# Performance work log

Measured on AMD Instinct MI355X. Metric: run time of the kernel, lower is better.

## Reference

```python
import jax, jax.numpy as jnp
import numpy as np

NUM_SCALES = 4
ENC = 64
KMAX = 16
DT = 0.005  # base_time_constant; original code's (undefined) self.dt interpreted as this


def setup_inputs() -> dict:
    key = jax.random.key(0)
    ks = jax.random.split(key, 5)
    events = jax.random.normal(ks[0], (2, 2, 32, 32, 64), dtype=jnp.float32)
    # matches torch.logspace(-3, -1, num_scales)
    time_constants = jnp.logspace(-3.0, -1.0, NUM_SCALES).astype(jnp.float32)
    temporal_kernels = jax.random.normal(ks[1], (NUM_SCALES, ENC, KMAX), dtype=jnp.float32)
    w1 = jax.random.normal(ks[2], (2 * NUM_SCALES, NUM_SCALES), dtype=jnp.float32) * 0.1
    b1 = jnp.zeros((2 * NUM_SCALES,), dtype=jnp.float32)
    w2 = jax.random.normal(ks[3], (NUM_SCALES, 2 * NUM_SCALES), dtype=jnp.float32) * 0.1
    b2 = jnp.zeros((NUM_SCALES,), dtype=jnp.float32)
    return {"events": events, "time_constants": time_constants,
            "temporal_kernels": temporal_kernels, "w1": w1, "b1": b1, "w2": w2, "b2": b2}


def reference(events, time_constants, temporal_kernels, w1, b1, w2, b2):
    B, C, H, W, T = events.shape
    k = min(KMAX, T)
    # decay kernels per scale: [S, k], normalized to sum 1
    t_idx = jnp.arange(k, dtype=jnp.float32)
    decay = jnp.exp(-t_idx[None, :] * DT / time_constants[:, None])
    decay = decay / decay.sum(axis=-1, keepdims=True)
    # combined learnable kernels: [S, E, k]
    combined = decay[:, None, :] * temporal_kernels[:, :, :k]

    Cf = C * H * W
    # one batched cross-correlation (torch F.conv1d semantics == lax conv, no flip)
    x = events.reshape(B * Cf, 1, T)                       # [B*Cf, 1, T]
    kern = combined.reshape(NUM_SCALES * ENC, 1, k)        # [S*E, 1, k]
    out = jax.lax.conv_general_dilated(
        x, kern, window_strides=(1,), padding=[(k // 2, k // 2)],
        dimension_numbers=("NCH", "OIH", "NCH"))           # [B*Cf, S*E, T+1]
    Tp = out.shape[-1]
    # [B, E, S, Cf, Tp] matching torch stack order (enc at dim1, scale at dim2)
    feats = out.reshape(B, Cf, NUM_SCALES, ENC, Tp).transpose(0, 3, 2, 1, 4)

    # torch .var() is unbiased -> ddof=1
    feature_variance = feats.var(axis=-1, ddof=1).mean(axis=(1, 3))  # [B, S]
    h = jax.nn.relu(feature_variance @ w1.T + b1)
    attn = jax.nn.softmax(h @ w2.T + b2, axis=-1)                    # [B, S]

    encoded = (feats * attn[:, None, :, None, None]).sum(axis=2)     # [B, E, Cf, Tp]
    return encoded
```

## Files before the change

### kernel.cpp

```cpp
#include <hip/hip_runtime.h>

#define CF 2048
#define TT 64
#define TP 65
#define KK 16
#define SS 4
#define EE 64
#define BB 2
#define DT_CONST 0.005f

typedef float f32x4 __attribute__((ext_vector_type(4)));
typedef short bf16x8 __attribute__((ext_vector_type(8)));


__global__ void __launch_bounds__(256, 2) kA_gram(const float* __restrict__ events,
                                                  float* __restrict__ ws) {
    __shared__ float xs[16][97];
    __shared__ float S1L[16][16];
    __shared__ float part[16][136];
    const int tid = threadIdx.x;
    const int bq  = blockIdx.x >> 7;

    {
        const float4* src = reinterpret_cast<const float4*>(
            events + (size_t)blockIdx.x * (16 * TT));
        float4 v = src[tid];
        int r = tid >> 4, c0 = ((tid & 15) << 2) + 8;
        xs[r][c0] = v.x; xs[r][c0+1] = v.y; xs[r][c0+2] = v.z; xs[r][c0+3] = v.w;
        for (int idx = tid; idx < 16 * 33; idx += 256) {
            int rr = idx / 33, k = idx % 33;
            int c = (k < 8) ? k : (k + 64);
            xs[rr][c] = 0.f;
        }
    }
    __syncthreads();

    const int r   = tid >> 4;
    const int lag = tid & 15;

    {
        float s = 0.f;
#pragma unroll
        for (int u = 0; u <= 64; ++u) s += xs[r][lag + u];
        S1L[r][lag] = s;
    }
    __syncthreads();

    {
        const float inv65 = 1.f / 65.f;
        float C = 0.f;
#pragma unroll
        for (int u = 0; u <= 64; ++u) C += xs[r][u] * xs[r][u + lag];
        part[r][lag] = C - S1L[r][0] * S1L[r][lag] * inv65;
#pragma unroll
        for (int d1 = 1; d1 <= 15; ++d1) {
            C += xs[r][64 + d1] * xs[r][64 + d1 + lag]
               - xs[r][d1 - 1]  * xs[r][d1 - 1 + lag];
            if (lag + d1 <= 15) {
                int p = 16 * d1 - ((d1 * (d1 - 1)) >> 1) + lag;
                part[r][p] = C - S1L[r][d1] * S1L[r][d1 + lag] * inv65;
            }
        }
    }
    __syncthreads();

    if (tid < 136) {
        float g = 0.f;
#pragma unroll
        for (int rr = 0; rr < 16; ++rr) g += part[rr][tid];
        ws[((size_t)(bq * 136 + tid)) * 128 + (blockIdx.x & 127)] = g;
    }
}

__global__ void __launch_bounds__(256, 2) kB3_main(
        const float* __restrict__ events, const float* __restrict__ tc,
        const float* __restrict__ tk, const float* __restrict__ w1,
        const float* __restrict__ b1, const float* __restrict__ w2,
        const float* __restrict__ b2, const float* __restrict__ ws,
        float* __restrict__ out) {
    __shared__ float U[5248];
    __shared__ float xs[8 * 97];
    __shared__ __align__(16) unsigned short wkbh[64 * 32];
    __shared__ __align__(16) unsigned short wkbl[64 * 32];
    __shared__ __align__(16) unsigned short BmatTh[80 * 24 + 16];
    __shared__ __align__(16) unsigned short BmatTl[80 * 24 + 16];
    float* Gf    = U;
    float* combL = U + 512;
    float* fvL   = U + 4608;
    const int tid = threadIdx.x;
    const int bid = blockIdx.x;
    const int b   = bid >> 8;

    for (int idx = tid; idx < 8 * 33; idx += 256) {
        int rr = idx / 33, k = idx % 33;
        int c = (k < 8) ? k : (k + 64);
        xs[rr * 97 + c] = 0.f;
    }
    if (tid < 128) {
        float4 v = reinterpret_cast<const float4*>(events + (size_t)bid * 512)[tid];
        int rr = tid >> 4, c0 = ((tid & 15) << 2) + 8;
        xs[rr * 97 + c0] = v.x; xs[rr * 97 + c0 + 1] = v.y;
        xs[rr * 97 + c0 + 2] = v.z; xs[rr * 97 + c0 + 3] = v.w;
    }
    for (int v = tid; v < 272; v += 256) {
        int b2 = (v >= 136) ? 1 : 0;
        int p  = v - b2 * 136;
        int pp = p, d1 = 0;
        while (pp >= KK - d1) { pp -= KK - d1; ++d1; }
        int d2 = d1 + pp;
        const float4* rp = reinterpret_cast<const float4*>(ws + (size_t)v * 128);
        float acc = 0.f;
#pragma unroll
        for (int i = 0; i < 32; ++i) { float4 q = rp[i]; acc += (q.x + q.y) + (q.z + q.w); }
        Gf[(b2 * KK + d1) * KK + d2] = acc;
        Gf[(b2 * KK + d2) * KK + d1] = acc;
    }
    {
        int s = tid >> 6;
        float inv = DT_CONST / tc[s];
        float dk[KK]; float dsum = 0.f;
#pragma unroll
        for (int j = 0; j < KK; ++j) { dk[j] = expf(-(float)j * inv); dsum += dk[j]; }
        float rn = 1.f / dsum;
#pragma unroll
        for (int i = 0; i < 4; ++i) {
            float4 v = reinterpret_cast<const float4*>(tk + tid * KK)[i];
            combL[tid * KK + 4*i + 0] = dk[4*i + 0] * rn * v.x;
            combL[tid * KK + 4*i + 1] = dk[4*i + 1] * rn * v.y;
            combL[tid * KK + 4*i + 2] = dk[4*i + 2] * rn * v.z;
            combL[tid * KK + 4*i + 3] = dk[4*i + 3] * rn * v.w;
        }
    }
    __syncthreads();

    {
        float c[KK];
#pragma unroll
        for (int i = 0; i < 4; ++i) {
            float4 v = reinterpret_cast<const float4*>(combL + tid * KK)[i];
            c[4*i] = v.x; c[4*i+1] = v.y; c[4*i+2] = v.z; c[4*i+3] = v.w;
        }
        float acc0 = 0.f, acc1 = 0.f;
#pragma unroll
        for (int d1 = 0; d1 < KK; ++d1) {
            float cd1 = c[d1];
            float t0 = 0.5f * Gf[d1 * KK + d1] * cd1;
            float t1 = 0.5f * Gf[256 + d1 * KK + d1] * cd1;
#pragma unroll
            for (int d2 = d1 + 1; d2 < KK; ++d2) {
                t0 += Gf[d1 * KK + d2] * c[d2];
                t1 += Gf[256 + d1 * KK + d2] * c[d2];
            }
            acc0 += 2.f * cd1 * t0;
            acc1 += 2.f * cd1 * t1;
        }
#pragma unroll
        for (int sft = 1; sft < 64; sft <<= 1) {
            acc0 += __shfl_xor(acc0, sft, 64);
            acc1 += __shfl_xor(acc1, sft, 64);
        }
        if ((tid & 63) == 0) {
            const float scale = 1.f / 8388608.f;
            fvL[(tid >> 6)]     = acc0 * scale;
            fvL[4 + (tid >> 6)] = acc1 * scale;
        }
    }
    __syncthreads();

    {
        float fv[SS];
#pragma unroll
        for (int s = 0; s < SS; ++s) fv[s] = fvL[b * SS + s];
        float h[8];
#pragma unroll
        for (int i = 0; i < 8; ++i) {
            float a = b1[i];
#pragma unroll
            for (int s = 0; s < SS; ++s) a += fv[s] * w1[i * SS + s];
            h[i] = a > 0.f ? a : 0.f;
        }
        float lg[SS]; float mx = -1e30f;
#pragma unroll
        for (int s = 0; s < SS; ++s) {
            float a = b2[s];
#pragma unroll
            for (int i = 0; i < 8; ++i) a += h[i] * w2[s * 8 + i];
            lg[s] = a; mx = fmaxf(mx, a);
        }
        float se = 0.f;
#pragma unroll
        for (int s = 0; s < SS; ++s) { lg[s] = expf(lg[s] - mx); se += lg[s]; }
        float attn[SS];
#pragma unroll
        for (int s = 0; s < SS; ++s) attn[s] = lg[s] / se;
#pragma unroll
        for (int j = 0; j < 4; ++j) {
            int idx = tid * 4 + j;
            int e = idx >> 4, k2 = idx & 15;
            float a = 0.f;
#pragma unroll
            for (int s = 0; s < SS; ++s)
                a += attn[s] * combL[(s * EE + e) * KK + k2];
            unsigned int bits = __float_as_uint(a);
            unsigned short hh = (unsigned short)(bits >> 16);
            float hf = __uint_as_float(((unsigned int)hh) << 16);
            unsigned short ll = (unsigned short)(__float_as_uint(a - hf) >> 16);
            wkbh[e * 32 + k2] = hh;      wkbl[e * 32 + k2] = ll;
            wkbh[e * 32 + 16 + k2] = 0;  wkbl[e * 32 + 16 + k2] = 0;
        }
    }
    __syncthreads();

    const int w   = tid >> 6;
    const int l   = tid & 63;
    const int llo = l & 15, lhi = l >> 4;
    bf16x8 Ah = *reinterpret_cast<const bf16x8*>(&wkbh[(w * 16 + llo) * 32 + 8 * lhi]);
    bf16x8 Al = *reinterpret_cast<const bf16x8*>(&wkbl[(w * 16 + llo) * 32 + 8 * lhi]);
    float* stage = U;
    const size_t obase0 = (size_t)b * 8519680 + (size_t)(bid & 255) * 520;

#pragma unroll 1
    for (int cf = 0; cf < 8; ++cf) {
        for (int idx = tid; idx < 1280; idx += 256) {
            int t = idx >> 4, k2 = idx & 15;
            float x = xs[cf * 97 + t + k2];
            unsigned int bits = __float_as_uint(x);
            unsigned short hh = (unsigned short)(bits >> 16);
            float hf = __uint_as_float(((unsigned int)hh) << 16);
            unsigned short ll = (unsigned short)(__float_as_uint(x - hf) >> 16);
            BmatTh[t * 24 + k2] = hh;
            BmatTl[t * 24 + k2] = ll;
        }
        __syncthreads();
#pragma unroll
        for (int nt = 0; nt < 5; ++nt) {
            bf16x8 Bh = *reinterpret_cast<const bf16x8*>(
                &BmatTh[(nt * 16 + llo) * 24 + 8 * lhi]);
            bf16x8 Bl = *reinterpret_cast<const bf16x8*>(
                &BmatTl[(nt * 16 + llo) * 24 + 8 * lhi]);
            f32x4 acc = {0.f, 0.f, 0.f, 0.f};
            acc = __builtin_amdgcn_mfma_f32_16x16x32_bf16(Al, Bh, acc, 0, 0, 0);
            acc = __builtin_amdgcn_mfma_f32_16x16x32_bf16(Ah, Bl, acc, 0, 0, 0);
            acc = __builtin_amdgcn_mfma_f32_16x16x32_bf16(Ah, Bh, acc, 0, 0, 0);
#pragma unroll
            for (int i = 0; i < 4; ++i)
                stage[(w * 16 + lhi * 4 + i) * 82 + nt * 16 + llo] = acc[i];
        }
        __syncthreads();
        {
            const size_t ob = obase0 + (size_t)cf * 65;
            int q = tid >> 6, t = tid & 63;
#pragma unroll
            for (int kk = 0; kk < 16; ++kk) {
                int e = q * 16 + kk;
                out[ob + (size_t)e * 133120 + t] = stage[e * 82 + t];
            }
            if (tid < 64) out[ob + (size_t)tid * 133120 + 64] = stage[tid * 82 + 64];
        }
        __syncthreads();
    }
}

extern "C" void kernel_launch(void* const* d_in, const int* in_sizes, int n_in,
                              void* d_out, int out_size, void* d_ws, size_t ws_size,
                              hipStream_t stream) {
    const float* events = (const float*)d_in[0];
    const float* tc     = (const float*)d_in[1];
    const float* tk     = (const float*)d_in[2];
    const float* w1     = (const float*)d_in[3];
    const float* b1     = (const float*)d_in[4];
    const float* w2     = (const float*)d_in[5];
    const float* b2     = (const float*)d_in[6];
    float* out = (float*)d_out;
    float* ws  = (float*)d_ws;

    hipLaunchKernelGGL(kA_gram,  dim3(256), dim3(256), 0, stream, events, ws);
    hipLaunchKernelGGL(kB3_main, dim3(512), dim3(256), 0, stream,
                       events, tc, tk, w1, b1, w2, b2, ws, out);
}
```

Before: 36.78 us.

## Split attention MLP into single-block kernel and spread conv over more blocks

Moves the Gram reduction, variance, MLP, softmax and attention-weighted kernel computation out of the main conv kernel into a single-block kernel. That kernel writes the bf16 hi/lo weight matrices to the workspace, so it runs once instead of being repeated in each of 512 blocks. The conv kernel now uses 2048 small blocks of two rows each and writes MFMA results straight to global memory instead of staging them through LDS. The Gram kernel doubles its thread count and splits each lag sum across lane pairs. This adds a third launch and a serial one-block kernel, and the direct stores are less coalesced.

```diff
diff --git a/kernel.cpp b/kernel.cpp
--- a/kernel.cpp
+++ b/kernel.cpp
@@ -1,8 +1,5 @@
 #include <hip/hip_runtime.h>
 
-#define CF 2048
-#define TT 64
-#define TP 65
 #define KK 16
 #define SS 4
 #define EE 64
@@ -12,53 +9,66 @@
 typedef float f32x4 __attribute__((ext_vector_type(4)));
 typedef short bf16x8 __attribute__((ext_vector_type(8)));
 
-
-__global__ void __launch_bounds__(256, 2) kA_gram(const float* __restrict__ events,
+#define WS_WK_F 34816
+
+__global__ void __launch_bounds__(512, 1) kA_gram(const float* __restrict__ events,
                                                   float* __restrict__ ws) {
     __shared__ float xs[16][97];
     __shared__ float S1L[16][16];
     __shared__ float part[16][136];
     const int tid = threadIdx.x;
-    const int bq  = blockIdx.x >> 7;
-
-    {
+
+    if (tid < 256) {
         const float4* src = reinterpret_cast<const float4*>(
-            events + (size_t)blockIdx.x * (16 * TT));
+            events + (size_t)blockIdx.x * 1024);
         float4 v = src[tid];
         int r = tid >> 4, c0 = ((tid & 15) << 2) + 8;
         xs[r][c0] = v.x; xs[r][c0+1] = v.y; xs[r][c0+2] = v.z; xs[r][c0+3] = v.w;
-        for (int idx = tid; idx < 16 * 33; idx += 256) {
-            int rr = idx / 33, k = idx % 33;
-            int c = (k < 8) ? k : (k + 64);
-            xs[rr][c] = 0.f;
-        }
-    }
-    __syncthreads();
-
-    const int r   = tid >> 4;
-    const int lag = tid & 15;
+    }
+    for (int idx = tid; idx < 16 * 33; idx += 512) {
+        int rr = idx / 33, k = idx % 33;
+        xs[rr][(k < 8) ? k : (k + 64)] = 0.f;
+    }
+    __syncthreads();
+
+    const int r   = tid >> 5;
+    const int c   = tid & 31;
+    const int lag = c >> 1;
+    const int h   = c & 1;
+    const int off = h * 33;
+    const float inv65 = 1.f / 65.f;
 
     {
         float s = 0.f;
 #pragma unroll
-        for (int u = 0; u <= 64; ++u) s += xs[r][lag + u];
-        S1L[r][lag] = s;
-    }
-    __syncthreads();
-
-    {
-        const float inv65 = 1.f / 65.f;
+        for (int j = 0; j < 32; ++j) s += xs[r][lag + off + j];
+        if (!h) s += xs[r][lag + 32];
+        s += __shfl_xor(s, 1, 64);
+        if (!h) S1L[r][lag] = s;
+    }
+    __syncthreads();
+
+    {
         float C = 0.f;
 #pragma unroll
-        for (int u = 0; u <= 64; ++u) C += xs[r][u] * xs[r][u + lag];
-        part[r][lag] = C - S1L[r][0] * S1L[r][lag] * inv65;
+        for (int j = 0; j < 32; ++j) C += xs[r][off + j] * xs[r][off + j + lag];
+        if (!h) C += xs[r][32] * xs[r][32 + lag];
+        {
+            float Ct = C + __shfl_xor(C, 1, 64);
+            if (!h) part[r][lag] = Ct - S1L[r][0] * S1L[r][lag] * inv65;
+        }
 #pragma unroll
         for (int d1 = 1; d1 <= 15; ++d1) {
-            C += xs[r][64 + d1] * xs[r][64 + d1 + lag]
-               - xs[r][d1 - 1]  * xs[r][d1 - 1 + lag];
+            const int add = d1 + off + 32 - h;
+            const int rem = d1 - 1 + off;
+            C += xs[r][add] * xs[r][add + lag] - xs[r][rem] * xs[r][rem + lag];
             if (lag + d1 <= 15) {
-                int p = 16 * d1 - ((d1 * (d1 - 1)) >> 1) + lag;
-                part[r][p] = C - S1L[r][d1] * S1L[r][d1 + lag] * inv65;
+                float Ct = C + __shfl_xor(C, 1, 64);
+                if (!h) {
+                    int p = 16 * d1 - ((d1 * (d1 - 1)) >> 1) + lag;
+                    part[r][p] = Ct - S1L[r][d1] * S1L[r][d1 + lag] * inv65;
+                }
+            } else {
             }
         }
     }
@@ -68,43 +78,23 @@
         float g = 0.f;
 #pragma unroll
         for (int rr = 0; rr < 16; ++rr) g += part[rr][tid];
-        ws[((size_t)(bq * 136 + tid)) * 128 + (blockIdx.x & 127)] = g;
-    }
-}
-
-__global__ void __launch_bounds__(256, 2) kB3_main(
-        const float* __restrict__ events, const float* __restrict__ tc,
+        ws[((size_t)((blockIdx.x >> 7) * 136 + tid)) * 128 + (blockIdx.x & 127)] = g;
+    }
+}
+
+__global__ void __launch_bounds__(256, 1) kM_mlp(const float* __restrict__ tc,
         const float* __restrict__ tk, const float* __restrict__ w1,
         const float* __restrict__ b1, const float* __restrict__ w2,
-        const float* __restrict__ b2, const float* __restrict__ ws,
-        float* __restrict__ out) {
-    __shared__ float U[5248];
-    __shared__ float xs[8 * 97];
-    __shared__ __align__(16) unsigned short wkbh[64 * 32];
-    __shared__ __align__(16) unsigned short wkbl[64 * 32];
-    __shared__ __align__(16) unsigned short BmatTh[80 * 24 + 16];
-    __shared__ __align__(16) unsigned short BmatTl[80 * 24 + 16];
-    float* Gf    = U;
-    float* combL = U + 512;
-    float* fvL   = U + 4608;
+        const float* __restrict__ b2, float* __restrict__ ws) {
+    __shared__ float Gf[2 * 256];
+    __shared__ float combL[SS * EE * KK];
+    __shared__ float fvL[BB * SS];
+    __shared__ float attnL[BB][SS];
     const int tid = threadIdx.x;
-    const int bid = blockIdx.x;
-    const int b   = bid >> 8;
-
-    for (int idx = tid; idx < 8 * 33; idx += 256) {
-        int rr = idx / 33, k = idx % 33;
-        int c = (k < 8) ? k : (k + 64);
-        xs[rr * 97 + c] = 0.f;
-    }
-    if (tid < 128) {
-        float4 v = reinterpret_cast<const float4*>(events + (size_t)bid * 512)[tid];
-        int rr = tid >> 4, c0 = ((tid & 15) << 2) + 8;
-        xs[rr * 97 + c0] = v.x; xs[rr * 97 + c0 + 1] = v.y;
-        xs[rr * 97 + c0 + 2] = v.z; xs[rr * 97 + c0 + 3] = v.w;
-    }
+
     for (int v = tid; v < 272; v += 256) {
-        int b2 = (v >= 136) ? 1 : 0;
-        int p  = v - b2 * 136;
+        int b = (v >= 136) ? 1 : 0;
+        int p = v - b * 136;
         int pp = p, d1 = 0;
         while (pp >= KK - d1) { pp -= KK - d1; ++d1; }
         int d2 = d1 + pp;
@@ -112,8 +102,8 @@
         float acc = 0.f;
 #pragma unroll
         for (int i = 0; i < 32; ++i) { float4 q = rp[i]; acc += (q.x + q.y) + (q.z + q.w); }
-        Gf[(b2 * KK + d1) * KK + d2] = acc;
-        Gf[(b2 * KK + d2) * KK + d1] = acc;
+        Gf[b * 256 + d1 * KK + d2] = acc;
+        Gf[b * 256 + d2 * KK + d1] = acc;
     }
     {
         int s = tid >> 6;
@@ -132,24 +122,23 @@
         }
     }
     __syncthreads();
-
-    {
-        float c[KK];
+    {
+        float cvec[KK];
 #pragma unroll
         for (int i = 0; i < 4; ++i) {
             float4 v = reinterpret_cast<const float4*>(combL + tid * KK)[i];
-            c[4*i] = v.x; c[4*i+1] = v.y; c[4*i+2] = v.z; c[4*i+3] = v.w;
+            cvec[4*i] = v.x; cvec[4*i+1] = v.y; cvec[4*i+2] = v.z; cvec[4*i+3] = v.w;
         }
         float acc0 = 0.f, acc1 = 0.f;
 #pragma unroll
         for (int d1 = 0; d1 < KK; ++d1) {
-            float cd1 = c[d1];
+            float cd1 = cvec[d1];
             float t0 = 0.5f * Gf[d1 * KK + d1] * cd1;
             float t1 = 0.5f * Gf[256 + d1 * KK + d1] * cd1;
 #pragma unroll
             for (int d2 = d1 + 1; d2 < KK; ++d2) {
-                t0 += Gf[d1 * KK + d2] * c[d2];
-                t1 += Gf[256 + d1 * KK + d2] * c[d2];
+                t0 += Gf[d1 * KK + d2] * cvec[d2];
+                t1 += Gf[256 + d1 * KK + d2] * cvec[d2];
             }
             acc0 += 2.f * cd1 * t0;
             acc1 += 2.f * cd1 * t1;
@@ -166,17 +155,14 @@
         }
     }
     __syncthreads();
-
-    {
-        float fv[SS];
-#pragma unroll
-        for (int s = 0; s < SS; ++s) fv[s] = fvL[b * SS + s];
+    if (tid < 2) {
+        int b = tid;
         float h[8];
 #pragma unroll
         for (int i = 0; i < 8; ++i) {
             float a = b1[i];
 #pragma unroll
-            for (int s = 0; s < SS; ++s) a += fv[s] * w1[i * SS + s];
+            for (int s = 0; s < SS; ++s) a += fvL[b * SS + s] * w1[i * SS + s];
             h[i] = a > 0.f ? a : 0.f;
         }
         float lg[SS]; float mx = -1e30f;
@@ -190,72 +176,92 @@
         float se = 0.f;
 #pragma unroll
         for (int s = 0; s < SS; ++s) { lg[s] = expf(lg[s] - mx); se += lg[s]; }
-        float attn[SS];
-#pragma unroll
-        for (int s = 0; s < SS; ++s) attn[s] = lg[s] / se;
-#pragma unroll
-        for (int j = 0; j < 4; ++j) {
-            int idx = tid * 4 + j;
-            int e = idx >> 4, k2 = idx & 15;
+#pragma unroll
+        for (int s = 0; s < SS; ++s) attnL[b][s] = lg[s] / se;
+    }
+    __syncthreads();
+    {
+        unsigned short* wkp = reinterpret_cast<unsigned short*>(ws + WS_WK_F);
+#pragma unroll
+        for (int j = 0; j < 8; ++j) {
+            int o = tid * 8 + j;
+            int b = o >> 10, e = (o >> 4) & 63, k = o & 15;
             float a = 0.f;
 #pragma unroll
             for (int s = 0; s < SS; ++s)
-                a += attn[s] * combL[(s * EE + e) * KK + k2];
+                a += attnL[b][s] * combL[(s * EE + e) * KK + k];
             unsigned int bits = __float_as_uint(a);
             unsigned short hh = (unsigned short)(bits >> 16);
             float hf = __uint_as_float(((unsigned int)hh) << 16);
             unsigned short ll = (unsigned short)(__float_as_uint(a - hf) >> 16);
-            wkbh[e * 32 + k2] = hh;      wkbl[e * 32 + k2] = ll;
-            wkbh[e * 32 + 16 + k2] = 0;  wkbl[e * 32 + 16 + k2] = 0;
-        }
-    }
-    __syncthreads();
-
-    const int w   = tid >> 6;
-    const int l   = tid & 63;
-    const int llo = l & 15, lhi = l >> 4;
-    bf16x8 Ah = *reinterpret_cast<const bf16x8*>(&wkbh[(w * 16 + llo) * 32 + 8 * lhi]);
-    bf16x8 Al = *reinterpret_cast<const bf16x8*>(&wkbl[(w * 16 + llo) * 32 + 8 * lhi]);
-    float* stage = U;
-    const size_t obase0 = (size_t)b * 8519680 + (size_t)(bid & 255) * 520;
+            int base = b * 2048 + e * 32 + k;
+            wkp[base]          = hh;   wkp[base + 16]        = 0;
+            wkp[4096 + base]   = ll;   wkp[4096 + base + 16] = 0;
+        }
+    }
+}
+
+__global__ void __launch_bounds__(256, 8) kC_conv(const float* __restrict__ events,
+                                                  const float* __restrict__ ws,
+                                                  float* __restrict__ out) {
+    __shared__ float xs[2][97];
+    __shared__ __align__(16) unsigned short Bh[80 * 24 + 16];
+    __shared__ __align__(16) unsigned short Bl[80 * 24 + 16];
+    const int tid = threadIdx.x;
+    const int bid = blockIdx.x;
+    const int b   = bid >> 10;
+    const int cf0 = (bid & 1023) << 1;
+    const int w   = tid >> 6, l = tid & 63, llo = l & 15, lhi = l >> 4;
+
+    for (int idx = tid; idx < 80 * 24 + 16; idx += 256) { Bh[idx] = 0; Bl[idx] = 0; }
+
+    const unsigned short* wkp = reinterpret_cast<const unsigned short*>(ws + WS_WK_F);
+    bf16x8 Ah = *reinterpret_cast<const bf16x8*>(wkp + b * 2048 + (w * 16 + llo) * 32 + 8 * lhi);
+    bf16x8 Al = *reinterpret_cast<const bf16x8*>(wkp + 4096 + b * 2048 + (w * 16 + llo) * 32 + 8 * lhi);
+
+    if (tid < 32) {
+        float4 v = reinterpret_cast<const float4*>(
+            events + ((size_t)b * 2048 + cf0) * 64)[tid];
+        int rr = tid >> 4, c0 = ((tid & 15) << 2) + 8;
+        xs[rr][c0] = v.x; xs[rr][c0+1] = v.y; xs[rr][c0+2] = v.z; xs[rr][c0+3] = v.w;
+    }
+    for (int idx = tid; idx < 66; idx += 256) {
+        int rr = idx / 33, k = idx % 33;
+        xs[rr][(k < 8) ? k : (k + 64)] = 0.f;
+    }
+    __syncthreads();
 
 #pragma unroll 1
-    for (int cf = 0; cf < 8; ++cf) {
-        for (int idx = tid; idx < 1280; idx += 256) {
-            int t = idx >> 4, k2 = idx & 15;
-            float x = xs[cf * 97 + t + k2];
+    for (int rr = 0; rr < 2; ++rr) {
+#pragma unroll
+        for (int q = 0; q < 5; ++q) {
+            int idx = tid + q * 256;
+            int t = idx >> 4, k = idx & 15;
+            float x = xs[rr][t + k];
             unsigned int bits = __float_as_uint(x);
             unsigned short hh = (unsigned short)(bits >> 16);
             float hf = __uint_as_float(((unsigned int)hh) << 16);
             unsigned short ll = (unsigned short)(__float_as_uint(x - hf) >> 16);
-            BmatTh[t * 24 + k2] = hh;
-            BmatTl[t * 24 + k2] = ll;
+            Bh[t * 24 + k] = hh;
+            Bl[t * 24 + k] = ll;
         }
         __syncthreads();
+
+        const size_t obase = ((size_t)(b * 64 + w * 16 + lhi * 4) * 2048 + (cf0 + rr)) * 65;
 #pragma unroll
         for (int nt = 0; nt < 5; ++nt) {
-            bf16x8 Bh = *reinterpret_cast<const bf16x8*>(
-                &BmatTh[(nt * 16 + llo) * 24 + 8 * lhi]);
-            bf16x8 Bl = *reinterpret_cast<const bf16x8*>(
-                &BmatTl[(nt * 16 + llo) * 24 + 8 * lhi]);
+            bf16x8 Xh = *reinterpret_cast<const bf16x8*>(Bh + (nt * 16 + llo) * 24 + 8 * lhi);
+            bf16x8 Xl = *reinterpret_cast<const bf16x8*>(Bl + (nt * 16 + llo) * 24 + 8 * lhi);
             f32x4 acc = {0.f, 0.f, 0.f, 0.f};
-            acc = __builtin_amdgcn_mfma_f32_16x16x32_bf16(Al, Bh, acc, 0, 0, 0);
-            acc = __builtin_amdgcn_mfma_f32_16x16x32_bf16(Ah, Bl, acc, 0, 0, 0);
-            acc = __builtin_amdgcn_mfma_f32_16x16x32_bf16(Ah, Bh, acc, 0, 0, 0);
-#pragma unroll
-            for (int i = 0; i < 4; ++i)
-                stage[(w * 16 + lhi * 4 + i) * 82 + nt * 16 + llo] = acc[i];
-        }
-        __syncthreads();
-        {
-            const size_t ob = obase0 + (size_t)cf * 65;
-            int q = tid >> 6, t = tid & 63;
-#pragma unroll
-            for (int kk = 0; kk < 16; ++kk) {
-                int e = q * 16 + kk;
-                out[ob + (size_t)e * 133120 + t] = stage[e * 82 + t];
+            acc = __builtin_amdgcn_mfma_f32_16x16x32_bf16(Al, Xh, acc, 0, 0, 0);
+            acc = __builtin_amdgcn_mfma_f32_16x16x32_bf16(Ah, Xl, acc, 0, 0, 0);
+            acc = __builtin_amdgcn_mfma_f32_16x16x32_bf16(Ah, Xh, acc, 0, 0, 0);
+            const int t0 = nt * 16 + llo;
+            if (t0 < 65) {
+#pragma unroll
+                for (int i = 0; i < 4; ++i)
+                    out[obase + (size_t)i * (2048 * 65) + t0] = acc[i];
             }
-            if (tid < 64) out[ob + (size_t)tid * 133120 + 64] = stage[tid * 82 + 64];
         }
         __syncthreads();
     }
@@ -274,7 +280,7 @@
     float* out = (float*)d_out;
     float* ws  = (float*)d_ws;
 
-    hipLaunchKernelGGL(kA_gram,  dim3(256), dim3(256), 0, stream, events, ws);
-    hipLaunchKernelGGL(kB3_main, dim3(512), dim3(256), 0, stream,
-                       events, tc, tk, w1, b1, w2, b2, ws, out);
-}
+    hipLaunchKernelGGL(kA_gram, dim3(256),  dim3(512), 0, stream, events, ws);
+    hipLaunchKernelGGL(kM_mlp,  dim3(1),    dim3(256), 0, stream, tc, tk, w1, b1, w2, b2, ws);
+    hipLaunchKernelGGL(kC_conv, dim3(2048), dim3(256), 0, stream, events, ws, out);
+}
```

Measured after the change: 37.95 us. 1.03x slower.
